# Performance work log

Measured on AMD Instinct MI355X. Metric: run time of the kernel, lower is better.

The kernel has to match this reference:

```python
import jax, jax.numpy as jnp
import numpy as np

ALPHA = 0.5
FILL = 0.1
EPS = 1e-8  # torch F.cosine_similarity eps

N_USERS = 8192
N_RECIPES = 8192  # must equal N_USERS to match torch broadcasting in column softmax
D = 64
B = 65536


def setup_inputs() -> dict:
    key = jax.random.key(0)
    k1, k2, k3, k4, k5, k6 = jax.random.split(key, 6)
    return {
        "user_embeddings": jax.random.normal(k1, (N_USERS, D), dtype=jnp.float32),
        "recipe_embeddings": jax.random.normal(k2, (N_RECIPES, D), dtype=jnp.float32),
        "ratings_scaled": jax.random.uniform(k3, (B,), dtype=jnp.float32),
        "cos_similarities_scaled": jax.random.uniform(k4, (B,), dtype=jnp.float32),
        "u_idx": jax.random.randint(k5, (B,), 0, N_USERS, dtype=jnp.int64 if jax.config.jax_enable_x64 else jnp.int32),
        "i_idx": jax.random.randint(k6, (B,), 0, N_RECIPES, dtype=jnp.int64 if jax.config.jax_enable_x64 else jnp.int32),
    }


def reference(user_embeddings, recipe_embeddings, ratings_scaled, cos_similarities_scaled, u_idx, i_idx):
    n, m = user_embeddings.shape[0], recipe_embeddings.shape[0]

    ratings_matrix = jnp.full((n, m), FILL, dtype=user_embeddings.dtype)
    ratings_matrix = ratings_matrix.at[u_idx, i_idx].set(ratings_scaled)

    # pairwise cosine similarity [n, m]
    num = user_embeddings @ recipe_embeddings.T
    u_norm = jnp.linalg.norm(user_embeddings, axis=1)    # [n]
    r_norm = jnp.linalg.norm(recipe_embeddings, axis=1)  # [m]
    denom = jnp.maximum(u_norm[:, None] * r_norm[None, :], EPS)
    cos = num / denom

    exp_cos = jnp.exp(cos)

    # row-normalized log-probs (softmax over recipes)
    log_probs_u = jnp.log(exp_cos / exp_cos.sum(axis=1, keepdims=True))
    loss_users = jnp.mean(-(log_probs_u * ratings_matrix).sum(axis=1))

    # column normalization, exactly as torch: sum(dim=0).view(-1,1) (requires n == m)
    col_sum = exp_cos.sum(axis=0).reshape(-1, 1)  # [m, 1]
    log_probs_r = jnp.log(exp_cos / col_sum)
    loss_recipes = jnp.mean(-(log_probs_r * ratings_matrix).sum(axis=0))

    contrastive = (loss_users + loss_recipes) / 2
    mse = jnp.mean((ratings_scaled - cos_similarities_scaled) ** 2)
    return ALPHA * contrastive + (1.0 - ALPHA) * mse
```

## Files before the change

### kernel.cpp

```cpp
#include <hip/hip_runtime.h>
#include <hip/hip_bf16.h>

#define N 8192
#define D 64
#define B_PAIRS 65536
#define FILL 0.1f
#define LOG2E 1.4426950408889634f
#define LN2 0.6931471805599453
#define RSP_STRIDE 36
#define CSP_STRIDE 65

typedef __attribute__((ext_vector_type(8))) short short8v;
typedef __attribute__((ext_vector_type(4))) float f32x4;

__device__ __forceinline__ float wave_reduce_sum(float v) {
  #pragma unroll
  for (int m = 1; m < 64; m <<= 1) v += __shfl_xor(v, m, 64);
  return v;
}

__device__ __forceinline__ float bf16_to_f32(unsigned short u) {
  unsigned int b = ((unsigned int)u) << 16;
  return __builtin_bit_cast(float, b);
}

__device__ __forceinline__ short f32_bf16_rne(float f) {
  unsigned int b = __builtin_bit_cast(unsigned int, f);
  return (short)((b + 0x7FFFu + ((b >> 16) & 1u)) >> 16);
}

__device__ __forceinline__ float fast_exp2(float x) {
#if __has_builtin(__builtin_amdgcn_exp2f)
  return __builtin_amdgcn_exp2f(x);
#else
  float r;
  asm("v_exp_f32 %0, %1\n\ts_nop 1" : "=v"(r) : "v"(x));
  return r;
#endif
}

__global__ __launch_bounds__(256) void norm_kernel(const float* __restrict__ U,
                                                   const float* __restrict__ R,
                                                   short* __restrict__ Ub,
                                                   short* __restrict__ Rb,
                                                   short* __restrict__ Ubp,
                                                   short* __restrict__ Rbp,
                                                   float* __restrict__ rowRMe,
                                                   float* __restrict__ sumU,
                                                   float* __restrict__ sumR,
                                                   double* __restrict__ scal) {
  const int t = threadIdx.x;
  const int b = blockIdx.x;
  if (b < 32) {
    rowRMe[b * 256 + t] = 0.f;
  } else if (b == 32) {
    if (t < 64) sumU[t] = 0.f;
    else if (t < 128) sumR[t - 64] = 0.f;
    else if (t < 136) scal[t - 128] = 0.0;
  }
  int row = b * 16 + (t >> 4);
  int c = t & 15;
  bool isU = row < N;
  int lrow = row & 15;
  const float* src = isU ? (U + (size_t)row * D) : (R + (size_t)(row - N) * D);
  float4 v = reinterpret_cast<const float4*>(src)[c];
  float ss = v.x * v.x + v.y * v.y + v.z * v.z + v.w * v.w;
  ss += __shfl_xor(ss, 1, 64);
  ss += __shfl_xor(ss, 2, 64);
  ss += __shfl_xor(ss, 4, 64);
  ss += __shfl_xor(ss, 8, 64);
  float scale = rsqrtf(ss) * (isU ? LOG2E : 1.0f);
  short4 o;
  o.x = f32_bf16_rne(v.x * scale);
  o.y = f32_bf16_rne(v.y * scale);
  o.z = f32_bf16_rne(v.z * scale);
  o.w = f32_bf16_rne(v.w * scale);
  int lrow_g = isU ? row : (row - N);
  short* dst = isU ? (Ub + (size_t)lrow_g * D) : (Rb + (size_t)lrow_g * D);
  reinterpret_cast<short4*>(dst)[c] = o;
  short* dst2 = isU ? Ubp : Rbp;
  size_t off2 = (size_t)(lrow_g >> 4) * 1024 +
                (size_t)(((c >> 3) * 64 + ((c >> 1) & 3) * 16 + lrow)) * 8 +
                (c & 1) * 4;
  *reinterpret_cast<short4*>(dst2 + off2) = o;
}

__global__ __launch_bounds__(256, 4) void mega_kernel(
    const short* __restrict__ Ub, const short* __restrict__ Rb,
    const short* __restrict__ Ubp, const short* __restrict__ Rbp,
    const float* __restrict__ ratings, const float* __restrict__ cossim,
    const int* __restrict__ u_idx, const int* __restrict__ i_idx,
    float* __restrict__ rowRMe, float* __restrict__ sumU,
    float* __restrict__ sumR, double* __restrict__ scal,
    float* __restrict__ rowpart, float* __restrict__ colpart) {
  __shared__ float lds_pool[128 * RSP_STRIDE + 16 * CSP_STRIDE];
  float* rsp = lds_pool;
  float* csp = lds_pool + 128 * RSP_STRIDE;
  float* sm  = lds_pool;
  const int bid = blockIdx.x;
  const int t = threadIdx.x;
  const int wid = t >> 6, lane = t & 63;

  if (bid >= 320) {
    const int g = bid - 320;
    const int cx = g & 63, by = g >> 6;
    const int wr = wid >> 1, wc = wid & 1;
    const int rowbase = by * 128 + wr * 64;
    const int colbase = cx * 128 + wc * 64;
    const int lrow = lane & 15;
    const int kgrp = lane >> 4;

    const short* Abase = Ubp + (size_t)(rowbase >> 4) * 1024 + (size_t)lane * 8;
    const short* Bbase = Rbp + (size_t)(colbase >> 4) * 1024 + (size_t)lane * 8;
    short8v aF[4][2], bF[4][2];
    #pragma unroll
    for (int m = 0; m < 4; ++m) {
      aF[m][0] = *reinterpret_cast<const short8v*>(Abase + m * 1024);
      bF[m][0] = *reinterpret_cast<const short8v*>(Bbase + m * 1024);
      aF[m][1] = *reinterpret_cast<const short8v*>(Abase + m * 1024 + 512);
      bF[m][1] = *reinterpret_cast<const short8v*>(Bbase + m * 1024 + 512);
    }

    float rowacc[4][4] = {};
    #pragma unroll
    for (int n = 0; n < 4; ++n) {
      f32x4 acc[4] = {};
      #pragma unroll
      for (int m = 0; m < 4; ++m)
        acc[m] = __builtin_amdgcn_mfma_f32_16x16x32_bf16(aF[m][0], bF[n][0], acc[m], 0, 0, 0);
      #pragma unroll
      for (int m = 0; m < 4; ++m)
        acc[m] = __builtin_amdgcn_mfma_f32_16x16x32_bf16(aF[m][1], bF[n][1], acc[m], 0, 0, 0);
      float p0 = 0.f, p1 = 0.f, p2 = 0.f, p3 = 0.f;
      #pragma unroll
      for (int r = 0; r < 4; ++r) {
        float e0 = fast_exp2(acc[0][r]); rowacc[0][r] += e0; p0 += e0;
        float e1 = fast_exp2(acc[1][r]); rowacc[1][r] += e1; p1 += e1;
        float e2 = fast_exp2(acc[2][r]); rowacc[2][r] += e2; p2 += e2;
        float e3 = fast_exp2(acc[3][r]); rowacc[3][r] += e3; p3 += e3;
      }
      csp[(wid * 4 + kgrp) * CSP_STRIDE + n * 16 + lrow] = (p0 + p1) + (p2 + p3);
    }

    #pragma unroll
    for (int m = 0; m < 4; ++m)
      #pragma unroll
      for (int r = 0; r < 4; ++r)
        rsp[(wr * 64 + m * 16 + kgrp * 4 + r) * RSP_STRIDE + wc * 16 + lrow] =
            rowacc[m][r];

    __syncthreads();

    if (t < 128) {
      const float4* rp4 = reinterpret_cast<const float4*>(&rsp[t * RSP_STRIDE]);
      float4 s0 = rp4[0], s1 = rp4[1], s2 = rp4[2], s3 = rp4[3];
      float4 s4 = rp4[4], s5 = rp4[5], s6 = rp4[6], s7 = rp4[7];
      float a0 = (s0.x + s0.y) + (s0.z + s0.w);
      float a1 = (s1.x + s1.y) + (s1.z + s1.w);
      float a2 = (s2.x + s2.y) + (s2.z + s2.w);
      float a3 = (s3.x + s3.y) + (s3.z + s3.w);
      float a4 = (s4.x + s4.y) + (s4.z + s4.w);
      float a5 = (s5.x + s5.y) + (s5.z + s5.w);
      float a6 = (s6.x + s6.y) + (s6.z + s6.w);
      float a7 = (s7.x + s7.y) + (s7.z + s7.w);
      rowpart[(size_t)cx * N + by * 128 + t] =
          ((a0 + a1) + (a2 + a3)) + ((a4 + a5) + (a6 + a7));
    } else {
      int c = t - 128;
      int half = c >> 6, c64 = c & 63;
      float csum = 0.f;
      #pragma unroll
      for (int kg = 0; kg < 4; ++kg) {
        csum += csp[(half * 4 + kg) * CSP_STRIDE + c64];
        csum += csp[((half + 2) * 4 + kg) * CSP_STRIDE + c64];
      }
      colpart[(size_t)by * N + cx * 128 + c] = csum;
    }

  } else if (bid < 256) {
    const int sb = bid;
    const int grp = lane >> 3, sub = lane & 7;
    float exacc = 0.f, msacc = 0.f;
    #pragma unroll 2
    for (int pass = 0; pass < 8; ++pass) {
      const int p = sb * 256 + pass * 32 + wid * 8 + grp;
      int u = u_idx[p], i = i_idx[p];
      short8v uv = *reinterpret_cast<const short8v*>(Ub + (size_t)u * D + sub * 8);
      short8v iv = *reinterpret_cast<const short8v*>(Rb + (size_t)i * D + sub * 8);
      float pd = 0.f;
      #pragma unroll
      for (int e = 0; e < 8; ++e)
        pd += bf16_to_f32((unsigned short)uv[e]) * bf16_to_f32((unsigned short)iv[e]);
      pd += __shfl_xor(pd, 1, 64);
      pd += __shfl_xor(pd, 2, 64);
      pd += __shfl_xor(pd, 4, 64);
      if (sub == 0) {
        float rv = ratings[p];
        exacc += (rv - FILL) * pd;
        float dd = rv - cossim[p];
        msacc += dd * dd;
        atomicAdd(&rowRMe[u], rv - FILL);
      }
    }
    exacc += __shfl_xor(exacc, 8, 64);
    exacc += __shfl_xor(exacc, 16, 64);
    exacc += __shfl_xor(exacc, 32, 64);
    msacc += __shfl_xor(msacc, 8, 64);
    msacc += __shfl_xor(msacc, 16, 64);
    msacc += __shfl_xor(msacc, 32, 64);
    if (lane == 0) { sm[wid] = exacc; sm[8 + wid] = msacc; }
    __syncthreads();
    if (t == 0)
      atomicAdd(&scal[1], (double)(sm[0] + sm[1] + sm[2] + sm[3]));
    else if (t == 64)
      atomicAdd(&scal[2], (double)(sm[8] + sm[9] + sm[10] + sm[11]));

  } else {
    int sb = bid - 256;
    const short* M = (sb < 32) ? Ub : Rb;
    float* dst = (sb < 32) ? sumU : sumR;
    int rbase = (sb & 31) * 256;
    float pc[8] = {};
    #pragma unroll
    for (int p = 0; p < 8; ++p) {
      int row = rbase + p * 32 + wid * 8 + (lane >> 3);
      short8v v = *reinterpret_cast<const short8v*>(M + (size_t)row * D + (lane & 7) * 8);
      #pragma unroll
      for (int e = 0; e < 8; ++e)
        pc[e] += bf16_to_f32((unsigned short)v[e]);
    }
    #pragma unroll
    for (int e = 0; e < 8; ++e) {
      pc[e] += __shfl_xor(pc[e], 8, 64);
      pc[e] += __shfl_xor(pc[e], 16, 64);
      pc[e] += __shfl_xor(pc[e], 32, 64);
    }
    if (lane < 8)
      #pragma unroll
      for (int e = 0; e < 8; ++e) sm[wid * 64 + lane * 8 + e] = pc[e];
    __syncthreads();
    if (t < 64)
      atomicAdd(&dst[t], sm[t] + sm[64 + t] + sm[128 + t] + sm[192 + t]);
  }
}

__global__ __launch_bounds__(256) void final_out_kernel(
    const float* __restrict__ rowpart, const float* __restrict__ colpart,
    const float* __restrict__ rowRMe, const float* __restrict__ sumU,
    const float* __restrict__ sumR, double* __restrict__ scal,
    float* __restrict__ out) {
  __shared__ float smr[256];
  __shared__ float smc[256];
  __shared__ unsigned int done;
  const int t = threadIdx.x;
  const int q = t >> 6, r = t & 63;
  const int i = blockIdx.x * 64 + r;
  float rsum = 0.f, csum = 0.f;
  #pragma unroll 8
  for (int p = q * 16; p < q * 16 + 16; ++p) {
    rsum += rowpart[(size_t)p * N + i];
    csum += colpart[(size_t)p * N + i];
  }
  smr[t] = rsum; smc[t] = csum;
  __syncthreads();
  if (t < 64) {
    rsum = smr[t] + smr[64 + t] + smr[128 + t] + smr[192 + t];
    csum = smc[t] + smc[64 + t] + smc[128 + t] + smc[192 + t];
    float term = (FILL * (float)N + rowRMe[i]) * 0.5f * (logf(rsum) + logf(csum));
    float s = wave_reduce_sum(term);
    if (t == 0) {
      atomicAdd(&scal[3], (double)s);
      __threadfence();
    }
  }
  __syncthreads();
  unsigned int* cnt = (unsigned int*)(scal + 7);
  if (t == 0) {
    __threadfence();
    done = atomicAdd(cnt, 1u);
  }
  __syncthreads();
  if (done == 127 && t < 64) {
    __threadfence();
    float p = sumU[t] * sumR[t];
    p = wave_reduce_sum(p);
    if (t == 0) {
      double T = (0.1 * (double)p + scal[1]) * LN2;
      double contrastive = (scal[3] - T) / (double)N;
      double mse = scal[2] / (double)B_PAIRS;
      out[0] = (float)(0.5 * contrastive + 0.5 * mse);
      *cnt = 0u;
    }
  }
}

extern "C" void kernel_launch(void* const* d_in, const int* in_sizes, int n_in,
                              void* d_out, int out_size, void* d_ws, size_t ws_size,
                              hipStream_t stream) {
  const float* U       = (const float*)d_in[0];
  const float* R       = (const float*)d_in[1];
  const float* ratings = (const float*)d_in[2];
  const float* cossim  = (const float*)d_in[3];
  const int*   u_idx   = (const int*)d_in[4];
  const int*   i_idx   = (const int*)d_in[5];

  float* ws      = (float*)d_ws;
  float* rowRMe  = ws;
  float* sumU    = ws + 8192;
  float* sumR    = ws + 8256;
  double* scal   = (double*)(ws + 8320);
  short* Ub      = (short*)(ws + 8448);
  short* Rb      = Ub + (size_t)N * D;
  float* rowpart = ws + 532736;
  float* colpart = ws + 1057024;
  short* Ubp     = (short*)(ws + 1581312);
  short* Rbp     = Ubp + (size_t)N * D;

  norm_kernel<<<(2 * N) / 16, 256, 0, stream>>>(U, R, Ub, Rb, Ubp, Rbp,
                                                rowRMe, sumU, sumR, scal);

  mega_kernel<<<4416, 256, 0, stream>>>(Ub, Rb, Ubp, Rbp, ratings, cossim,
                                        u_idx, i_idx, rowRMe, sumU, sumR, scal,
                                        rowpart, colpart);

  final_out_kernel<<<128, 256, 0, stream>>>(rowpart, colpart, rowRMe,
                                            sumU, sumR, scal, (float*)d_out);
}
```

Measured before the change: 39.50 us.

## Enlarge GEMM block tile to 128x512 and write column partials directly per wave

Each GEMM block now covers 128 rows by 512 columns, looping over four column chunks while keeping the A fragments in registers. This cuts the block count from 4416 to 1344 and lowers the number of rowpart partials from 64 to 16 per row. Column sums are reduced within the wave by shuffles and stored straight to colpart, which removes the shared-memory column staging. In exchange there are twice as many colpart partials (128 per column) for the final kernel to sum, and fewer blocks means less parallelism and latency hiding per block.

```diff
diff --git a/kernel.cpp b/kernel.cpp
--- a/kernel.cpp
+++ b/kernel.cpp
@@ -8,7 +8,6 @@
 #define LOG2E 1.4426950408889634f
 #define LN2 0.6931471805599453
 #define RSP_STRIDE 36
-#define CSP_STRIDE 65
 
 typedef __attribute__((ext_vector_type(8))) short short8v;
 typedef __attribute__((ext_vector_type(4))) float f32x4;
@@ -93,53 +92,66 @@
     float* __restrict__ rowRMe, float* __restrict__ sumU,
     float* __restrict__ sumR, double* __restrict__ scal,
     float* __restrict__ rowpart, float* __restrict__ colpart) {
-  __shared__ float lds_pool[128 * RSP_STRIDE + 16 * CSP_STRIDE];
-  float* rsp = lds_pool;
-  float* csp = lds_pool + 128 * RSP_STRIDE;
-  float* sm  = lds_pool;
+  __shared__ float rsp[128 * RSP_STRIDE];
+  float* sm = rsp;
   const int bid = blockIdx.x;
   const int t = threadIdx.x;
   const int wid = t >> 6, lane = t & 63;
 
   if (bid >= 320) {
     const int g = bid - 320;
-    const int cx = g & 63, by = g >> 6;
+    const int by = g >> 4;
+    const int cx = g & 15;
     const int wr = wid >> 1, wc = wid & 1;
-    const int rowbase = by * 128 + wr * 64;
-    const int colbase = cx * 128 + wc * 64;
     const int lrow = lane & 15;
     const int kgrp = lane >> 4;
 
-    const short* Abase = Ubp + (size_t)(rowbase >> 4) * 1024 + (size_t)lane * 8;
-    const short* Bbase = Rbp + (size_t)(colbase >> 4) * 1024 + (size_t)lane * 8;
-    short8v aF[4][2], bF[4][2];
+    const short8v* Uv = reinterpret_cast<const short8v*>(Ubp);
+    const short8v* Rv = reinterpret_cast<const short8v*>(Rbp);
+
+    short8v aF[4][2];
     #pragma unroll
     for (int m = 0; m < 4; ++m) {
-      aF[m][0] = *reinterpret_cast<const short8v*>(Abase + m * 1024);
-      bF[m][0] = *reinterpret_cast<const short8v*>(Bbase + m * 1024);
-      aF[m][1] = *reinterpret_cast<const short8v*>(Abase + m * 1024 + 512);
-      bF[m][1] = *reinterpret_cast<const short8v*>(Bbase + m * 1024 + 512);
+      size_t tA = (size_t)(by * 8 + wr * 4 + m) * 128 + lane;
+      aF[m][0] = Uv[tA];
+      aF[m][1] = Uv[tA + 64];
     }
 
     float rowacc[4][4] = {};
-    #pragma unroll
-    for (int n = 0; n < 4; ++n) {
-      f32x4 acc[4] = {};
-      #pragma unroll
-      for (int m = 0; m < 4; ++m)
-        acc[m] = __builtin_amdgcn_mfma_f32_16x16x32_bf16(aF[m][0], bF[n][0], acc[m], 0, 0, 0);
-      #pragma unroll
-      for (int m = 0; m < 4; ++m)
-        acc[m] = __builtin_amdgcn_mfma_f32_16x16x32_bf16(aF[m][1], bF[n][1], acc[m], 0, 0, 0);
-      float p0 = 0.f, p1 = 0.f, p2 = 0.f, p3 = 0.f;
-      #pragma unroll
-      for (int r = 0; r < 4; ++r) {
-        float e0 = fast_exp2(acc[0][r]); rowacc[0][r] += e0; p0 += e0;
-        float e1 = fast_exp2(acc[1][r]); rowacc[1][r] += e1; p1 += e1;
-        float e2 = fast_exp2(acc[2][r]); rowacc[2][r] += e2; p2 += e2;
-        float e3 = fast_exp2(acc[3][r]); rowacc[3][r] += e3; p3 += e3;
+
+    #pragma unroll 1
+    for (int ci = 0; ci < 4; ++ci) {
+      short8v bF[4][2];
+      #pragma unroll
+      for (int n = 0; n < 4; ++n) {
+        size_t tB = (size_t)(cx * 32 + ci * 8 + wc * 4 + n) * 128 + lane;
+        bF[n][0] = Rv[tB];
+        bF[n][1] = Rv[tB + 64];
       }
-      csp[(wid * 4 + kgrp) * CSP_STRIDE + n * 16 + lrow] = (p0 + p1) + (p2 + p3);
+      #pragma unroll
+      for (int n = 0; n < 4; ++n) {
+        f32x4 acc[4] = {};
+        #pragma unroll
+        for (int m = 0; m < 4; ++m)
+          acc[m] = __builtin_amdgcn_mfma_f32_16x16x32_bf16(aF[m][0], bF[n][0], acc[m], 0, 0, 0);
+        #pragma unroll
+        for (int m = 0; m < 4; ++m)
+          acc[m] = __builtin_amdgcn_mfma_f32_16x16x32_bf16(aF[m][1], bF[n][1], acc[m], 0, 0, 0);
+        float p0 = 0.f, p1 = 0.f, p2 = 0.f, p3 = 0.f;
+        #pragma unroll
+        for (int r = 0; r < 4; ++r) {
+          float e0 = fast_exp2(acc[0][r]); rowacc[0][r] += e0; p0 += e0;
+          float e1 = fast_exp2(acc[1][r]); rowacc[1][r] += e1; p1 += e1;
+          float e2 = fast_exp2(acc[2][r]); rowacc[2][r] += e2; p2 += e2;
+          float e3 = fast_exp2(acc[3][r]); rowacc[3][r] += e3; p3 += e3;
+        }
+        float cacc = (p0 + p1) + (p2 + p3);
+        cacc += __shfl_xor(cacc, 16, 64);
+        cacc += __shfl_xor(cacc, 32, 64);
+        if (lane < 16)
+          colpart[(size_t)(by * 2 + wr) * N +
+                  cx * 512 + ci * 128 + wc * 64 + n * 16 + lane] = cacc;
+      }
     }
 
     #pragma unroll
@@ -148,7 +160,6 @@
       for (int r = 0; r < 4; ++r)
         rsp[(wr * 64 + m * 16 + kgrp * 4 + r) * RSP_STRIDE + wc * 16 + lrow] =
             rowacc[m][r];
-
     __syncthreads();
 
     if (t < 128) {
@@ -165,16 +176,6 @@
       float a7 = (s7.x + s7.y) + (s7.z + s7.w);
       rowpart[(size_t)cx * N + by * 128 + t] =
           ((a0 + a1) + (a2 + a3)) + ((a4 + a5) + (a6 + a7));
-    } else {
-      int c = t - 128;
-      int half = c >> 6, c64 = c & 63;
-      float csum = 0.f;
-      #pragma unroll
-      for (int kg = 0; kg < 4; ++kg) {
-        csum += csp[(half * 4 + kg) * CSP_STRIDE + c64];
-        csum += csp[((half + 2) * 4 + kg) * CSP_STRIDE + c64];
-      }
-      colpart[(size_t)by * N + cx * 128 + c] = csum;
     }
 
   } else if (bid < 256) {
@@ -256,11 +257,10 @@
   const int q = t >> 6, r = t & 63;
   const int i = blockIdx.x * 64 + r;
   float rsum = 0.f, csum = 0.f;
+  #pragma unroll
+  for (int p = q * 4; p < q * 4 + 4; ++p) rsum += rowpart[(size_t)p * N + i];
   #pragma unroll 8
-  for (int p = q * 16; p < q * 16 + 16; ++p) {
-    rsum += rowpart[(size_t)p * N + i];
-    csum += colpart[(size_t)p * N + i];
-  }
+  for (int p = q * 32; p < q * 32 + 32; ++p) csum += colpart[(size_t)p * N + i];
   smr[t] = rsum; smc[t] = csum;
   __syncthreads();
   if (t < 64) {
@@ -312,14 +312,14 @@
   short* Ub      = (short*)(ws + 8448);
   short* Rb      = Ub + (size_t)N * D;
   float* rowpart = ws + 532736;
-  float* colpart = ws + 1057024;
-  short* Ubp     = (short*)(ws + 1581312);
+  float* colpart = ws + 663808;
+  short* Ubp     = (short*)(ws + 1712384);
   short* Rbp     = Ubp + (size_t)N * D;
 
   norm_kernel<<<(2 * N) / 16, 256, 0, stream>>>(U, R, Ub, Rb, Ubp, Rbp,
                                                 rowRMe, sumU, sumR, scal);
 
-  mega_kernel<<<4416, 256, 0, stream>>>(Ub, Rb, Ubp, Rbp, ratings, cossim,
+  mega_kernel<<<1344, 256, 0, stream>>>(Ub, Rb, Ubp, Rbp, ratings, cossim,
                                         u_idx, i_idx, rowRMe, sumU, sumR, scal,
                                         rowpart, colpart);
 
```

After: 57.48 us. +45.5%, slower.
